# Performance work log

Hardware: AMD Instinct MI355X
Metric: run time of the kernel (lower is better)

## Reference

```python
import jax, jax.numpy as jnp
import numpy as np

B, C, H, W = 8, 256, 128, 128
P = 7          # patch_size (odd)
N = 500        # n_infer (eval mode)
HIDDEN = C // 16  # reduction=16


def setup_inputs() -> dict:
    key = jax.random.key(0)
    ks = jax.random.split(key, 8)
    def s(k, shape, fan_in):
        return jax.random.normal(k, shape, jnp.float32) * (1.0 / np.sqrt(fan_in))
    return {
        "x_main": jax.random.normal(ks[0], (B, C, H, W), jnp.float32),
        "x_aux": jax.random.normal(ks[1], (B, C, H, W), jnp.float32),
        "scorer_w": s(ks[2], (C,), C),            # 1x1 conv C->1
        "scorer_b": s(ks[3], (1,), C),
        "fc1_w": s(ks[4], (3 * C, HIDDEN), 3 * C),
        "fc1_b": jnp.zeros((HIDDEN,), jnp.float32),
        "fc2_w": s(ks[5], (HIDDEN, C), HIDDEN),
        "fc2_b": jnp.zeros((C,), jnp.float32),
        "proj_w": s(ks[6], (C, C), C),
        "proj_b": jnp.zeros((C,), jnp.float32),
        "n": N,
    }


def _sample_patch_feats(feat, px, py):
    # feat: [C,H,W]; px,py: [n,p,p] pixel coords (align_corners=False convention).
    # Bilinear sample with zero padding, then pool 0.5*(mean+max) over the patch.
    c, h, w = feat.shape
    x0 = jnp.floor(px); y0 = jnp.floor(py)
    wx1 = px - x0; wy1 = py - y0
    def gather(yi, xi):
        valid = ((yi >= 0) & (yi < h) & (xi >= 0) & (xi < w)).astype(feat.dtype)
        yc = jnp.clip(yi, 0, h - 1).astype(jnp.int32)
        xc = jnp.clip(xi, 0, w - 1).astype(jnp.int32)
        return feat[:, yc, xc] * valid  # [C,n,p,p]
    patch = (gather(y0, x0) * ((1 - wy1) * (1 - wx1))
             + gather(y0, x0 + 1) * ((1 - wy1) * wx1)
             + gather(y0 + 1, x0) * (wy1 * (1 - wx1))
             + gather(y0 + 1, x0 + 1) * (wy1 * wx1))  # [C,n,p,p]
    v = 0.5 * (patch.mean(axis=(2, 3)) + patch.max(axis=(2, 3)))  # [C,n]
    return v.T  # [n,C]


def reference(x_main, x_aux, scorer_w, scorer_b, fc1_w, fc1_b, fc2_w, fc2_b, proj_w, proj_b, n):
    b, c, h, w = x_main.shape
    # saliency scores -> topk indices over flattened HW
    score = jax.nn.sigmoid(jnp.einsum('bchw,c->bhw', x_main, scorer_w) + scorer_b[0])
    score = score.reshape(b, h * w)
    _, idx = jax.lax.top_k(score, n)  # [b,n] int32
    idx_y = idx // w
    idx_x = idx - idx_y * w
    # build the (clamped) normalized grid exactly as the torch module does,
    # then convert to pixel coords: px = ((g+1)*W - 1)/2 (align_corners=False)
    r = P // 2
    d = jnp.arange(-r, r + 1, dtype=jnp.float32)
    yy, xx = jnp.meshgrid(d, d, indexing='ij')
    off_x = xx * (2.0 / w); off_y = yy * (2.0 / h)           # [p,p]
    cx = (idx_x.astype(jnp.float32) + 0.5) * (2.0 / w) - 1.0  # [b,n]
    cy = (idx_y.astype(jnp.float32) + 0.5) * (2.0 / h) - 1.0
    gx = jnp.clip(cx[:, :, None, None] + off_x, -1.0, 1.0)    # [b,n,p,p]
    gy = jnp.clip(cy[:, :, None, None] + off_y, -1.0, 1.0)
    px = ((gx + 1.0) * w - 1.0) * 0.5
    py = ((gy + 1.0) * h - 1.0) * 0.5
    sample = jax.vmap(_sample_patch_feats)
    v_main = sample(x_main, px, py)  # [b,n,C]
    v_aux = sample(x_aux, px, py)    # aux_in_proj is Identity (c_main==c_aux)
    # instance-level cross attention
    sim = jnp.einsum('bnc,bmc->bnm', v_main, v_aux) / jnp.sqrt(jnp.float32(c))
    attn = jax.nn.softmax(sim, axis=-1)
    v_hat = jnp.einsum('bnm,bmc->bnc', attn, v_aux)
    # gated fusion MLP
    z = jnp.concatenate([v_main, v_hat, v_main - v_hat], axis=-1)  # [b,n,3C]
    gate = jax.nn.sigmoid(jax.nn.relu(z @ fc1_w + fc1_b) @ fc2_w + fc2_b)
    v_fused = v_main + gate * (v_main - v_hat)
    v_inj = v_fused @ proj_w + proj_b  # [b,n,C]
    # scatter-add reinjection at the topk locations
    inject = jnp.zeros((b, h * w, c), x_main.dtype)
    inject = inject.at[jnp.arange(b)[:, None], idx].add(v_inj)
    inject = inject.reshape(b, h, w, c).transpose(0, 3, 1, 2)
    return x_main + inject
```

## Files before the change

### kernel.cpp

```cpp
#include <hip/hip_runtime.h>
#include <cstdint>
#include <cstddef>

#define HW    16384
#define CCH   256
#define WID   128
#define NB    8
#define NSEL  500
#define NPAD  512
#define CPG   8

__device__ __forceinline__ unsigned key_of(float f) {
  unsigned u = __float_as_uint(f);
  return (u & 0x80000000u) ? ~u : (u | 0x80000000u);
}

__global__ __launch_bounds__(256) void score_kernel(const float* __restrict__ x,
                                                    const float* __restrict__ w,
                                                    float* __restrict__ logits) {
  __shared__ float ws[CCH];
  int tid = threadIdx.x;
  ws[tid] = w[tid];
  __syncthreads();
  int pix = blockIdx.x * 256 + tid;
  int b = pix >> 14, p = pix & (HW - 1);
  const float* xp = x + ((size_t)b << 22) + p;
  float acc = 0.f;
#pragma unroll 16
  for (int c = 0; c < CCH; c++) acc += xp[(size_t)c * HW] * ws[c];
  logits[pix] = acc;
}

__global__ __launch_bounds__(1024) void topk_kernel(const float* __restrict__ logits,
                                                    int* __restrict__ idx_out,
                                                    int* __restrict__ map) {
  int b = blockIdx.x, tid = threadIdx.x;
  const float* lg = logits + (size_t)b * HW;
  __shared__ unsigned hist[256];
  __shared__ unsigned sscan[1024];
  __shared__ unsigned bc_prefix;
  __shared__ int bc_want;
  __shared__ int cnt;

  unsigned kreg[16];
#pragma unroll
  for (int j = 0; j < 4; j++) {
    float4 v = *(const float4*)&lg[tid * 16 + j * 4];
    kreg[4 * j + 0] = key_of(v.x);
    kreg[4 * j + 1] = key_of(v.y);
    kreg[4 * j + 2] = key_of(v.z);
    kreg[4 * j + 3] = key_of(v.w);
  }
  for (int p = tid; p < HW; p += 1024) map[(size_t)b * HW + p] = -1;

  unsigned prefix = 0;
  int want = NSEL;
  for (int shift = 24; shift >= 0; shift -= 8) {
    if (tid < 256) hist[tid] = 0;
    __syncthreads();
#pragma unroll
    for (int j = 0; j < 16; j++) {
      unsigned u = kreg[j];
      bool m = (shift == 24) || ((u >> (shift + 8)) == (prefix >> (shift + 8)));
      if (m) atomicAdd(&hist[(u >> shift) & 255u], 1u);
    }
    __syncthreads();
    unsigned h = (tid < 256) ? hist[tid] : 0u;
    if (tid < 256) sscan[tid] = h;
    __syncthreads();
    for (int o = 1; o < 256; o <<= 1) {
      unsigned v = (tid < 256 && tid + o < 256) ? sscan[tid + o] : 0u;
      __syncthreads();
      if (tid < 256) sscan[tid] += v;
      __syncthreads();
    }
    if (tid < 256) {
      unsigned above = sscan[tid] - h;
      if ((int)sscan[tid] >= want && (int)above < want) {
        bc_prefix = prefix | ((unsigned)tid << shift);
        bc_want = want - (int)above;
      }
    }
    __syncthreads();
    prefix = bc_prefix;
    want = bc_want;
    __syncthreads();
  }
  unsigned thr = prefix;

  int local = 0;
#pragma unroll
  for (int j = 0; j < 16; j++) local += (kreg[j] == thr) ? 1 : 0;
  sscan[tid] = (unsigned)local;
  if (tid == 0) cnt = 0;
  __syncthreads();
  for (int o = 1; o < 1024; o <<= 1) {
    unsigned v = (tid >= o) ? sscan[tid - o] : 0u;
    __syncthreads();
    sscan[tid] += v;
    __syncthreads();
  }
  int rank = (int)sscan[tid] - local;
#pragma unroll
  for (int j = 0; j < 16; j++) {
    unsigned u = kreg[j];
    bool take = (u > thr);
    if (u == thr) { if (rank < want) take = true; rank++; }
    if (take) {
      int s = atomicAdd(&cnt, 1);
      int p = tid * 16 + j;
      idx_out[b * NPAD + s] = p;
      map[(size_t)b * HW + p] = s;
    }
  }
}

__device__ __forceinline__ void patch_weights(int p, int* xc, int* yc, float* wx, float* wy) {
  int iy = p >> 7, ix = p & (WID - 1);
#pragma unroll
  for (int d = 0; d < 7; d++) {
    int t = ix + d - 3;
    bool in = (t >= 0) && (t < WID);
    xc[d] = in ? t : (t < 0 ? 0 : WID - 1);
    wx[d] = in ? 1.f : 0.5f;
    t = iy + d - 3;
    in = (t >= 0) && (t < WID);
    yc[d] = in ? t : (t < 0 ? 0 : WID - 1);
    wy[d] = in ? 1.f : 0.5f;
  }
}

__global__ __launch_bounds__(512, 4) void gather_pipe_kernel(const float* __restrict__ xm,
                                                             const float* __restrict__ xa,
                                                             const int* __restrict__ idx,
                                                             float* __restrict__ vmainT,
                                                             float* __restrict__ vauxT) {
  extern __shared__ float plane[];
  int g = blockIdx.x, b = blockIdx.y, z = blockIdx.z;
  int tid = threadIdx.x;
  int c0 = g * CPG;
  const float* src = (z == 0 ? xm : xa) + ((size_t)(b * CCH + c0)) * HW;
  float* dst = (z == 0 ? vmainT : vauxT) + (((size_t)(b * CCH + c0)) << 9);

  int t500 = (tid < NSEL) ? tid : 0;
  int p = idx[b * NPAD + t500];
  float wx[7], wy[7];
  int xc[7], yc[7], rb[7];
  patch_weights(p, xc, yc, wx, wy);
#pragma unroll
  for (int d = 0; d < 7; d++) rb[d] = yc[d] * WID;

  float4 r[8];
#pragma unroll
  for (int j = 0; j < 8; j++) r[j] = *(const float4*)&src[(size_t)(tid + j * 512) * 4];
#pragma unroll
  for (int j = 0; j < 8; j++) *(float4*)&plane[(tid + j * 512) * 4] = r[j];
  __syncthreads();

  for (int c = 0; c < CPG; c++) {
    if (c + 1 < CPG) {
      const float* s2 = src + (size_t)(c + 1) * HW;
#pragma unroll
      for (int j = 0; j < 8; j++) r[j] = *(const float4*)&s2[(size_t)(tid + j * 512) * 4];
    }
    if (tid < NSEL) {
      float s = 0.f, mx = -INFINITY;
#pragma unroll
      for (int dy = 0; dy < 7; dy++) {
        float rs = 0.f, rm = -INFINITY;
        int rbb = rb[dy];
#pragma unroll
        for (int dx = 0; dx < 7; dx++) {
          float v = plane[rbb + xc[dx]] * wx[dx];
          rs += v;
          rm = fmaxf(rm, v);
        }
        s += rs * wy[dy];
        mx = fmaxf(mx, rm * wy[dy]);
      }
      dst[((size_t)c << 9) + tid] = 0.5f * (s * (1.f / 49.f) + mx);
    } else {
      dst[((size_t)c << 9) + tid] = 0.f;
    }
    if (c + 1 < CPG) {
      __syncthreads();
#pragma unroll
      for (int j = 0; j < 8; j++) *(float4*)&plane[(tid + j * 512) * 4] = r[j];
      __syncthreads();
    }
  }
}

template <int M, int N, int K, bool AT, bool BT, bool BSHARED, int EPI>
__global__ __launch_bounds__(256) void gemm_kernel(const float* __restrict__ A,
                                                   const float* __restrict__ B,
                                                   float* __restrict__ C,
                                                   const float* __restrict__ bias) {
  constexpr int BM = 64, BN = 64, BK = 16;
  __shared__ float As[BK][BM + 4];
  __shared__ float Bs[BK][BN + 4];
  int tid = threadIdx.x;
  int bx = blockIdx.x, by = blockIdx.y, b = blockIdx.z;
  const float* Ab = A + (size_t)b * M * K;
  const float* Bb = BSHARED ? B : (B + (size_t)b * ((size_t)K * N));
  int tx = tid & 15, ty = tid >> 4;
  float acc[4][4] = {};

  for (int k0 = 0; k0 < K; k0 += BK) {
    if (!AT) {
      int ar = tid >> 2, ac4 = (tid & 3) * 4;
      const float4 av = *(const float4*)&Ab[(size_t)(by * BM + ar) * K + k0 + ac4];
      As[ac4 + 0][ar] = av.x; As[ac4 + 1][ar] = av.y;
      As[ac4 + 2][ar] = av.z; As[ac4 + 3][ar] = av.w;
    } else {
      int kr = tid >> 4, mc = (tid & 15) * 4;
      *(float4*)&As[kr][mc] = *(const float4*)&Ab[(size_t)(k0 + kr) * M + by * BM + mc];
    }
    if (!BT) {
      int br = tid >> 4, bc4 = (tid & 15) * 4;
      *(float4*)&Bs[br][bc4] = *(const float4*)&Bb[(size_t)(k0 + br) * N + bx * BN + bc4];
    } else {
      int nr = tid >> 2, kc4 = (tid & 3) * 4;
      const float4 bv = *(const float4*)&Bb[(size_t)(bx * BN + nr) * K + k0 + kc4];
      Bs[kc4 + 0][nr] = bv.x; Bs[kc4 + 1][nr] = bv.y;
      Bs[kc4 + 2][nr] = bv.z; Bs[kc4 + 3][nr] = bv.w;
    }
    __syncthreads();
#pragma unroll
    for (int kk = 0; kk < BK; kk++) {
      const float4 a = *(const float4*)&As[kk][ty * 4];
      const float4 bb = *(const float4*)&Bs[kk][tx * 4];
      float av[4] = {a.x, a.y, a.z, a.w};
      float bv[4] = {bb.x, bb.y, bb.z, bb.w};
#pragma unroll
      for (int rr = 0; rr < 4; rr++)
#pragma unroll
        for (int ss = 0; ss < 4; ss++) acc[rr][ss] += av[rr] * bv[ss];
    }
    __syncthreads();
  }
  if (EPI == 2) {
#pragma unroll
    for (int s = 0; s < 4; s++) {
      int col = bx * BN + tx * 4 + s;
      float bv = bias[col];
#pragma unroll
      for (int r = 0; r < 4; r++) {
        int row = by * BM + ty * 4 + r;
        C[((size_t)b * N + col) * M + row] = acc[r][s] + bv;
      }
    }
  } else {
    float scale = (EPI == 1) ? 0.0625f : 1.f;
#pragma unroll
    for (int r = 0; r < 4; r++) {
      int row = by * BM + ty * 4 + r;
#pragma unroll
      for (int s = 0; s < 4; s++) {
        int col = bx * BN + tx * 4 + s;
        C[((size_t)b * M + row) * N + col] = acc[r][s] * scale;
      }
    }
  }
}

__global__ __launch_bounds__(256) void softmax_kernel(float* __restrict__ sim) {
  int i = blockIdx.x, b = blockIdx.y, tid = threadIdx.x;
  float* row = sim + ((size_t)b * NPAD + i) * NPAD;
  float v0 = (tid < NSEL) ? row[tid] : -INFINITY;
  int j1 = tid + 256;
  float v1 = (j1 < NSEL) ? row[j1] : -INFINITY;
  float m = fmaxf(v0, v1);
  for (int o = 32; o; o >>= 1) m = fmaxf(m, __shfl_down(m, o));
  __shared__ float red[4];
  __shared__ float bm, bs;
  int wave = tid >> 6, lane = tid & 63;
  if (lane == 0) red[wave] = m;
  __syncthreads();
  if (tid == 0) bm = fmaxf(fmaxf(red[0], red[1]), fmaxf(red[2], red[3]));
  __syncthreads();
  m = bm;
  float e0 = (tid < NSEL) ? expf(v0 - m) : 0.f;
  float e1 = (j1 < NSEL) ? expf(v1 - m) : 0.f;
  float s = e0 + e1;
  for (int o = 32; o; o >>= 1) s += __shfl_down(s, o);
  if (lane == 0) red[wave] = s;
  __syncthreads();
  if (tid == 0) bs = 1.f / (red[0] + red[1] + red[2] + red[3]);
  __syncthreads();
  row[tid] = e0 * bs;
  row[j1] = e1 * bs;
}

__global__ __launch_bounds__(256) void mlp_kernel(const float* __restrict__ vmainT,
                                                  const float* __restrict__ vhat,
                                                  const float* __restrict__ fc1w,
                                                  const float* __restrict__ fc1b,
                                                  const float* __restrict__ fc2w,
                                                  const float* __restrict__ fc2b,
                                                  float* __restrict__ vfused) {
  int i = blockIdx.x, b = blockIdx.y, c = threadIdx.x;
  size_t base = ((size_t)b * NPAD + i) * CCH + c;
  float vm = vmainT[(((size_t)(b * CCH + c)) << 9) + i];
  float vh = vhat[base], vd = vm - vh;
  const float* w0 = fc1w + (size_t)c * 16;
  const float* w1 = fc1w + (size_t)(256 + c) * 16;
  const float* w2 = fc1w + (size_t)(512 + c) * 16;
  float ph[16];
#pragma unroll
  for (int k = 0; k < 16; k++) ph[k] = vm * w0[k] + vh * w1[k] + vd * w2[k];
#pragma unroll
  for (int o = 32; o; o >>= 1)
#pragma unroll
    for (int k = 0; k < 16; k++) ph[k] += __shfl_down(ph[k], o);
  __shared__ float red[4][16];
  __shared__ float hsh[16];
  int wave = c >> 6, lane = c & 63;
  if (lane == 0)
#pragma unroll
    for (int k = 0; k < 16; k++) red[wave][k] = ph[k];
  __syncthreads();
  if (c < 16) {
    float s = red[0][c] + red[1][c] + red[2][c] + red[3][c] + fc1b[c];
    hsh[c] = fmaxf(s, 0.f);
  }
  __syncthreads();
  float g = fc2b[c];
#pragma unroll
  for (int k = 0; k < 16; k++) g += hsh[k] * fc2w[k * 256 + c];
  g = 1.f / (1.f + expf(-g));
  vfused[base] = vm + g * vd;
}

__global__ __launch_bounds__(256) void final_kernel(const float* __restrict__ x,
                                                    const int* __restrict__ map,
                                                    const float* __restrict__ vinjT,
                                                    float* __restrict__ out) {
  int gid = blockIdx.x * 256 + threadIdx.x;
  int p4 = gid & 4095;
  int c = (gid >> 12) & 255;
  int b = gid >> 20;
  size_t xoff = (((size_t)(b * 256 + c)) << 14) + ((size_t)p4 << 2);
  float4 xv = *(const float4*)(x + xoff);
  const int4 mv = *(const int4*)(map + ((size_t)b << 14) + (p4 << 2));
  const float* vt = vinjT + ((size_t)(b * 256 + c) << 9);
  if (mv.x >= 0) xv.x += vt[mv.x];
  if (mv.y >= 0) xv.y += vt[mv.y];
  if (mv.z >= 0) xv.z += vt[mv.z];
  if (mv.w >= 0) xv.w += vt[mv.w];
  *(float4*)(out + xoff) = xv;
}

extern "C" void kernel_launch(void* const* d_in, const int* in_sizes, int n_in,
                              void* d_out, int out_size, void* d_ws, size_t ws_size,
                              hipStream_t stream) {
  const float* x_main   = (const float*)d_in[0];
  const float* x_aux    = (const float*)d_in[1];
  const float* scorer_w = (const float*)d_in[2];
  const float* fc1_w = (const float*)d_in[4];
  const float* fc1_b = (const float*)d_in[5];
  const float* fc2_w = (const float*)d_in[6];
  const float* fc2_b = (const float*)d_in[7];
  const float* proj_w = (const float*)d_in[8];
  const float* proj_b = (const float*)d_in[9];
  (void)in_sizes; (void)n_in; (void)out_size; (void)ws_size;

  float* ws = (float*)d_ws;
  float* logits = ws;
  int*   idx    = (int*)(ws + 131072);
  int*   map    = (int*)(ws + 135168);
  float* vmainT = ws + 266240;
  float* vauxT  = ws + 1314816;
  float* vhat   = ws + 2363392;
  float* vfused = ws + 3411968;
  float* sim    = ws + 4460544;
  float* vinjT  = vhat;
  float* out = (float*)d_out;

  score_kernel<<<512, 256, 0, stream>>>(x_main, scorer_w, logits);
  topk_kernel<<<NB, 1024, 0, stream>>>(logits, idx, map);
  gather_pipe_kernel<<<dim3(CCH / CPG, NB, 2), 512, HW * sizeof(float), stream>>>(
      x_main, x_aux, idx, vmainT, vauxT);
  gemm_kernel<NPAD, NPAD, CCH, true, false, false, 1>
      <<<dim3(8, 8, NB), 256, 0, stream>>>(vmainT, vauxT, sim, nullptr);
  softmax_kernel<<<dim3(NPAD, NB), 256, 0, stream>>>(sim);
  gemm_kernel<NPAD, CCH, NPAD, false, true, false, 0>
      <<<dim3(4, 8, NB), 256, 0, stream>>>(sim, vauxT, vhat, nullptr);
  mlp_kernel<<<dim3(NPAD, NB), 256, 0, stream>>>(vmainT, vhat, fc1_w, fc1_b,
                                                 fc2_w, fc2_b, vfused);
  gemm_kernel<NPAD, CCH, CCH, false, false, true, 2>
      <<<dim3(4, 8, NB), 256, 0, stream>>>(vfused, proj_w, vinjT, proj_b);
  final_kernel<<<32768, 256, 0, stream>>>(x_main, map, vinjT, out);
}
```

Measured before the change: 591.1 us.

## Double-buffer gather planes via direct global-to-LDS loads, shuffle-based top-k scans

The patch-gather kernel now streams each channel plane straight into LDS with global_load_lds into a double buffer, replacing the register staging. This aims to overlap the next plane's load with the current plane's patch pooling and to drop one barrier per channel. Channels per block go from 8 to 16, so there are half as many blocks and each uses twice the LDS. That costs occupancy. The top-k histogram and rank scans now use wave shuffles instead of barrier-heavy shared-memory scans, and the MLP's first-layer reduction moves from cross-lane shuffles to a shared-memory transpose sum.

```diff
diff --git a/kernel.cpp b/kernel.cpp
--- a/kernel.cpp
+++ b/kernel.cpp
@@ -8,7 +8,7 @@
 #define NB    8
 #define NSEL  500
 #define NPAD  512
-#define CPG   8
+#define CPG   16
 
 __device__ __forceinline__ unsigned key_of(float f) {
   unsigned u = __float_as_uint(f);
@@ -35,9 +35,11 @@
                                                     int* __restrict__ idx_out,
                                                     int* __restrict__ map) {
   int b = blockIdx.x, tid = threadIdx.x;
+  int lane = tid & 63, wave = tid >> 6;
   const float* lg = logits + (size_t)b * HW;
   __shared__ unsigned hist[256];
-  __shared__ unsigned sscan[1024];
+  __shared__ unsigned wtot[4];
+  __shared__ unsigned wsum[16];
   __shared__ unsigned bc_prefix;
   __shared__ int bc_want;
   __shared__ int cnt;
@@ -66,17 +68,19 @@
     }
     __syncthreads();
     unsigned h = (tid < 256) ? hist[tid] : 0u;
-    if (tid < 256) sscan[tid] = h;
-    __syncthreads();
-    for (int o = 1; o < 256; o <<= 1) {
-      unsigned v = (tid < 256 && tid + o < 256) ? sscan[tid + o] : 0u;
-      __syncthreads();
-      if (tid < 256) sscan[tid] += v;
-      __syncthreads();
-    }
+    unsigned v = h;
+#pragma unroll
+    for (int o = 1; o < 64; o <<= 1) {
+      unsigned t = __shfl_down(v, o);
+      if (lane < 64 - o) v += t;
+    }
+    if (tid < 256 && lane == 0) wtot[wave] = v;
+    __syncthreads();
     if (tid < 256) {
-      unsigned above = sscan[tid] - h;
-      if ((int)sscan[tid] >= want && (int)above < want) {
+      unsigned sfx = v;
+      for (int w2 = wave + 1; w2 < 4; w2++) sfx += wtot[w2];
+      unsigned above = sfx - h;
+      if ((int)sfx >= want && (int)above < want) {
         bc_prefix = prefix | ((unsigned)tid << shift);
         bc_want = want - (int)above;
       }
@@ -84,23 +88,24 @@
     __syncthreads();
     prefix = bc_prefix;
     want = bc_want;
-    __syncthreads();
   }
   unsigned thr = prefix;
 
   int local = 0;
 #pragma unroll
   for (int j = 0; j < 16; j++) local += (kreg[j] == thr) ? 1 : 0;
-  sscan[tid] = (unsigned)local;
+  unsigned pv = (unsigned)local;
+#pragma unroll
+  for (int o = 1; o < 64; o <<= 1) {
+    unsigned t = __shfl_up(pv, o);
+    if (lane >= o) pv += t;
+  }
+  if (lane == 63) wsum[wave] = pv;
   if (tid == 0) cnt = 0;
   __syncthreads();
-  for (int o = 1; o < 1024; o <<= 1) {
-    unsigned v = (tid >= o) ? sscan[tid - o] : 0u;
-    __syncthreads();
-    sscan[tid] += v;
-    __syncthreads();
-  }
-  int rank = (int)sscan[tid] - local;
+  unsigned woff = 0;
+  for (int w2 = 0; w2 < wave; w2++) woff += wsum[w2];
+  int rank = (int)(woff + pv) - local;
 #pragma unroll
   for (int j = 0; j < 16; j++) {
     unsigned u = kreg[j];
@@ -130,12 +135,12 @@
   }
 }
 
-__global__ __launch_bounds__(512, 4) void gather_pipe_kernel(const float* __restrict__ xm,
-                                                             const float* __restrict__ xa,
-                                                             const int* __restrict__ idx,
-                                                             float* __restrict__ vmainT,
-                                                             float* __restrict__ vauxT) {
-  extern __shared__ float plane[];
+__global__ __launch_bounds__(512) void gather_dma_kernel(const float* __restrict__ xm,
+                                                         const float* __restrict__ xa,
+                                                         const int* __restrict__ idx,
+                                                         float* __restrict__ vmainT,
+                                                         float* __restrict__ vauxT) {
+  extern __shared__ float plane2[];
   int g = blockIdx.x, b = blockIdx.y, z = blockIdx.z;
   int tid = threadIdx.x;
   int c0 = g * CPG;
@@ -150,18 +155,27 @@
 #pragma unroll
   for (int d = 0; d < 7; d++) rb[d] = yc[d] * WID;
 
-  float4 r[8];
-#pragma unroll
-  for (int j = 0; j < 8; j++) r[j] = *(const float4*)&src[(size_t)(tid + j * 512) * 4];
-#pragma unroll
-  for (int j = 0; j < 8; j++) *(float4*)&plane[(tid + j * 512) * 4] = r[j];
+#pragma unroll
+  for (int j = 0; j < 8; j++) {
+    int off = (tid + j * 512) * 4;
+    __builtin_amdgcn_global_load_lds(
+        (const __attribute__((address_space(1))) float*)(src + off),
+        (__attribute__((address_space(3))) float*)(plane2 + off), 16, 0, 0);
+  }
   __syncthreads();
 
   for (int c = 0; c < CPG; c++) {
+    float* cur = plane2 + ((c & 1) ? HW : 0);
+    float* nxt = plane2 + ((c & 1) ? 0 : HW);
     if (c + 1 < CPG) {
       const float* s2 = src + (size_t)(c + 1) * HW;
 #pragma unroll
-      for (int j = 0; j < 8; j++) r[j] = *(const float4*)&s2[(size_t)(tid + j * 512) * 4];
+      for (int j = 0; j < 8; j++) {
+        int off = (tid + j * 512) * 4;
+        __builtin_amdgcn_global_load_lds(
+            (const __attribute__((address_space(1))) float*)(s2 + off),
+            (__attribute__((address_space(3))) float*)(nxt + off), 16, 0, 0);
+      }
     }
     if (tid < NSEL) {
       float s = 0.f, mx = -INFINITY;
@@ -169,25 +183,21 @@
       for (int dy = 0; dy < 7; dy++) {
         float rs = 0.f, rm = -INFINITY;
         int rbb = rb[dy];
+        float wyd = wy[dy];
 #pragma unroll
         for (int dx = 0; dx < 7; dx++) {
-          float v = plane[rbb + xc[dx]] * wx[dx];
+          float v = cur[rbb + xc[dx]] * wx[dx];
           rs += v;
           rm = fmaxf(rm, v);
         }
-        s += rs * wy[dy];
-        mx = fmaxf(mx, rm * wy[dy]);
+        s += rs * wyd;
+        mx = fmaxf(mx, rm * wyd);
       }
       dst[((size_t)c << 9) + tid] = 0.5f * (s * (1.f / 49.f) + mx);
     } else {
       dst[((size_t)c << 9) + tid] = 0.f;
     }
-    if (c + 1 < CPG) {
-      __syncthreads();
-#pragma unroll
-      for (int j = 0; j < 8; j++) *(float4*)&plane[(tid + j * 512) * 4] = r[j];
-      __syncthreads();
-    }
+    __syncthreads();
   }
 }
 
@@ -306,30 +316,30 @@
   const float* w0 = fc1w + (size_t)c * 16;
   const float* w1 = fc1w + (size_t)(256 + c) * 16;
   const float* w2 = fc1w + (size_t)(512 + c) * 16;
-  float ph[16];
-#pragma unroll
-  for (int k = 0; k < 16; k++) ph[k] = vm * w0[k] + vh * w1[k] + vd * w2[k];
-#pragma unroll
-  for (int o = 32; o; o >>= 1)
-#pragma unroll
-    for (int k = 0; k < 16; k++) ph[k] += __shfl_down(ph[k], o);
-  __shared__ float red[4][16];
+  __shared__ float ph[256][17];
+  __shared__ float part2[16][17];
   __shared__ float hsh[16];
-  int wave = c >> 6, lane = c & 63;
-  if (lane == 0)
-#pragma unroll
-    for (int k = 0; k < 16; k++) red[wave][k] = ph[k];
+#pragma unroll
+  for (int k = 0; k < 16; k++) ph[c][k] = vm * w0[k] + vh * w1[k] + vd * w2[k];
+  __syncthreads();
+  int kk = c & 15, g = c >> 4;
+  float part = 0.f;
+#pragma unroll
+  for (int j = 0; j < 16; j++) part += ph[g * 16 + j][kk];
+  part2[g][kk] = part;
   __syncthreads();
   if (c < 16) {
-    float s = red[0][c] + red[1][c] + red[2][c] + red[3][c] + fc1b[c];
+    float s = fc1b[c];
+#pragma unroll
+    for (int g2 = 0; g2 < 16; g2++) s += part2[g2][c];
     hsh[c] = fmaxf(s, 0.f);
   }
   __syncthreads();
-  float g = fc2b[c];
-#pragma unroll
-  for (int k = 0; k < 16; k++) g += hsh[k] * fc2w[k * 256 + c];
-  g = 1.f / (1.f + expf(-g));
-  vfused[base] = vm + g * vd;
+  float gte = fc2b[c];
+#pragma unroll
+  for (int k = 0; k < 16; k++) gte += hsh[k] * fc2w[k * 256 + c];
+  gte = 1.f / (1.f + expf(-gte));
+  vfused[base] = vm + gte * vd;
 }
 
 __global__ __launch_bounds__(256) void final_kernel(const float* __restrict__ x,
@@ -379,7 +389,7 @@
 
   score_kernel<<<512, 256, 0, stream>>>(x_main, scorer_w, logits);
   topk_kernel<<<NB, 1024, 0, stream>>>(logits, idx, map);
-  gather_pipe_kernel<<<dim3(CCH / CPG, NB, 2), 512, HW * sizeof(float), stream>>>(
+  gather_dma_kernel<<<dim3(CCH / CPG, NB, 2), 512, 2 * HW * sizeof(float), stream>>>(
       x_main, x_aux, idx, vmainT, vauxT);
   gemm_kernel<NPAD, NPAD, CCH, true, false, false, 1>
       <<<dim3(8, 8, NB), 256, 0, stream>>>(vmainT, vauxT, sim, nullptr);
```

Result: faster. 488.7 us (-17.3%).
